# Performance work log

Measured on AMD Instinct MI355X. Metric: run time of the kernel, lower is better.

## Reference

```python
import jax, jax.numpy as jnp
import numpy as np

N, E = 50000, 800000
CUR, HID, OUT = 128, 96, 128
NEG_SLOPE = 0.01  # F.leaky_relu default


def setup_inputs() -> dict:
    key = jax.random.key(0)
    ks = jax.random.split(key, 12)
    inv = lambda d: 1.0 / np.sqrt(d)
    return {
        "h": jax.random.normal(ks[0], (N, CUR), jnp.float32),
        "x": jax.random.normal(ks[1], (N, CUR), jnp.float32),
        "edge_index": jax.random.randint(ks[2], (2, E), 0, N, dtype=jnp.int64),
        "edge_weight": jax.random.uniform(ks[3], (E,), jnp.float32),
        # preprocessor_x: Linear(cur_dim, hidden_dim)
        "pre_W": jax.random.uniform(ks[4], (CUR, HID), jnp.float32, -inv(CUR), inv(CUR)),
        "pre_b": jax.random.uniform(ks[5], (HID,), jnp.float32, -inv(CUR), inv(CUR)),
        # SAGEConv(hidden, out): lin_l (neighbor, with bias) + lin_r (root, no bias)
        "sage_Wl": jax.random.uniform(ks[6], (HID, OUT), jnp.float32, -inv(HID), inv(HID)),
        "sage_bl": jnp.zeros((OUT,), jnp.float32),
        "sage_Wr": jax.random.uniform(ks[7], (HID, OUT), jnp.float32, -inv(HID), inv(HID)),
        # ARMAConv(hidden, out) with K=1 stacks, T=1 layers (PyG defaults)
        "arma_W": jax.random.uniform(ks[8], (HID, OUT), jnp.float32, -inv(HID), inv(HID)),
        "arma_V": jax.random.uniform(ks[9], (HID, OUT), jnp.float32, -inv(HID), inv(HID)),
        "arma_b": jnp.zeros((OUT,), jnp.float32),
    }


def _cell(x, src, dst, edge_weight, pre_W, pre_b,
          sage_Wl, sage_bl, sage_Wr, arma_W, arma_V, arma_b):
    n = x.shape[0]
    xh = x @ pre_W + pre_b  # [N, HID]

    # ---- SAGEConv: mean aggregation of edge-weighted neighbor features ----
    msg = xh[src] * edge_weight[:, None]                     # [E, HID]
    aggr = jax.ops.segment_sum(msg, dst, num_segments=n)     # [N, HID]
    cnt = jax.ops.segment_sum(jnp.ones_like(edge_weight), dst, num_segments=n)
    mean = aggr / jnp.maximum(cnt, 1.0)[:, None]
    o_sage = mean @ sage_Wl + sage_bl + xh @ sage_Wr         # [N, OUT]

    # ---- ARMAConv (K=1, T=1): ReLU(L_hat (x W) + x V + b) ----
    deg = jax.ops.segment_sum(edge_weight, dst, num_segments=n)
    dinv = jnp.where(deg > 0, jax.lax.rsqrt(jnp.maximum(deg, 1e-30)), 0.0)
    norm = dinv[src] * edge_weight * dinv[dst]               # [E]
    xw = xh @ arma_W                                         # [N, OUT]
    prop = jax.ops.segment_sum(xw[src] * norm[:, None], dst, num_segments=n)
    o_arma = jax.nn.relu(prop + xh @ arma_V + arma_b)        # [N, OUT]

    o1 = jax.nn.leaky_relu(o_sage, NEG_SLOPE)
    o2 = jax.nn.leaky_relu(o_arma, NEG_SLOPE)
    return jax.nn.relu(o1 + o2)


def reference(h, x, edge_index, edge_weight, pre_W, pre_b,
              sage_Wl, sage_bl, sage_Wr, arma_W, arma_V, arma_b):
    src, dst = edge_index[0], edge_index[1]
    his = x
    o3 = _cell(x, src, dst, edge_weight, pre_W, pre_b,
               sage_Wl, sage_bl, sage_Wr, arma_W, arma_V, arma_b)
    return (his, o3)
```

## Files before the change

### kernel.cpp

```cpp
#include <hip/hip_runtime.h>


typedef __attribute__((ext_vector_type(8))) short bf16x8;
typedef __attribute__((ext_vector_type(4))) float f32x4;

__device__ __forceinline__ float bf2f(unsigned short u) {
    return __uint_as_float(((unsigned)u) << 16);
}
__device__ __forceinline__ unsigned short f2bf(float f) {
    unsigned u = __float_as_uint(f);
    return (unsigned short)((u + 0x7FFFu + ((u >> 16) & 1u)) >> 16);
}

__device__ __forceinline__ int edge_src(const int* ei, int e, int E, int flag) {
    return flag ? ei[2 * e] : ei[e];
}
__device__ __forceinline__ int edge_dst(const int* ei, int e, int E, int flag) {
    return flag ? ei[2 * (E + e)] : ei[E + e];
}

__global__ void k_wprep(const unsigned* __restrict__ eiu,
                        const float* __restrict__ Wl, const float* __restrict__ Wr,
                        const float* __restrict__ Wa, const float* __restrict__ Va,
                        const float* __restrict__ preW,
                        unsigned short* __restrict__ Wf_s,
                        unsigned short* __restrict__ Wf_a,
                        unsigned short* __restrict__ Wfp,
                        int* __restrict__ flag,
                        int4* __restrict__ cnt4, int nz4) {
    if (blockIdx.x == 0) {
        __shared__ int bad;
        if (threadIdx.x == 0) bad = 0;
        __syncthreads();
        int nb = 0;
#pragma unroll
        for (int q = 0; q < 4; q++) {
            unsigned w = eiu[2 * (threadIdx.x * 4 + q) + 1];
            if (w != 0) nb++;
        }
        if (nb) atomicAdd(&bad, nb);
        __syncthreads();
        if (threadIdx.x == 0) *flag = (bad == 0) ? 1 : 0;
        return;
    }
    int tid = (blockIdx.x - 1) * blockDim.x + threadIdx.x;
    if (tid < 6144) {
        int mat = tid / 3072, rem = tid % 3072;
        int kstep = rem / 512, rem2 = rem % 512;
        int g = rem2 / 128, j = rem2 % 128;
        int k0 = kstep * 32 + g * 8;
        const float* Wtop = mat ? Wa : Wl;
        const float* Wbot = mat ? Va : Wr;
        unsigned short* dst = (mat ? Wf_a : Wf_s) + (((size_t)(kstep * 4 + g) * 128 + j) * 8);
#pragma unroll
        for (int kk = 0; kk < 8; kk++) {
            int k = k0 + kk;
            float v = (k < 96) ? Wtop[k * 128 + j] : Wbot[(k - 96) * 128 + j];
            dst[kk] = f2bf(v);
        }
    } else if (tid < 7680) {
        int rem = tid - 6144;
        int kstep = rem / 384, rem2 = rem % 384;
        int g = rem2 / 96, j = rem2 % 96;
        int k0 = kstep * 32 + g * 8;
        unsigned short* dst = Wfp + (((size_t)(kstep * 4 + g) * 96 + j) * 8);
#pragma unroll
        for (int kk = 0; kk < 8; kk++) dst[kk] = f2bf(preW[(k0 + kk) * 96 + j]);
    } else if (tid >= 8192 && tid < 8192 + nz4) {
        cnt4[tid - 8192] = make_int4(0, 0, 0, 0);
    }
}

__global__ __launch_bounds__(256) void k_xh_count(
    const float* __restrict__ x, const unsigned short* __restrict__ Wfp,
    const float* __restrict__ b, unsigned short* __restrict__ xhbf,
    float* __restrict__ out0, int N, int xhBlocks,
    const int* __restrict__ ei, int* __restrict__ cntS, int* __restrict__ pos,
    int E, const int* __restrict__ flagp) {
    __shared__ unsigned short X[64][136];
    if (blockIdx.x >= xhBlocks) {
        int e = (blockIdx.x - xhBlocks) * 256 + threadIdx.x;
        if (e < E) {
            int flag = *flagp;
            int d = edge_dst(ei, e, E, flag);
            int shard = blockIdx.x & 7;
            int lp = atomicAdd(&cntS[(size_t)shard * N + d], 1);
            pos[e] = (lp << 3) | shard;
        }
        return;
    }
    int t = threadIdx.x;
    int nb = blockIdx.x * 64;
    for (int u = t; u < 2048; u += 256) {
        int row = u >> 5, q = u & 31;
        long gn = nb + row;
        float4 v = make_float4(0.f, 0.f, 0.f, 0.f);
        if (gn < N) {
            v = ((const float4*)(x + gn * 128))[q];
            ((float4*)(out0 + gn * 128))[q] = v;
        }
        unsigned short* p = &X[row][q * 4];
        p[0] = f2bf(v.x); p[1] = f2bf(v.y); p[2] = f2bf(v.z); p[3] = f2bf(v.w);
    }
    __syncthreads();
    int lane = t & 63, w = t >> 6;
    int lr = lane & 15, lg = lane >> 4;
    bf16x8 a[4];
#pragma unroll
    for (int ks = 0; ks < 4; ks++)
        a[ks] = *(const bf16x8*)&X[w * 16 + lr][ks * 32 + lg * 8];
    for (int jt = 0; jt < 6; jt++) {
        f32x4 acc = {0.f, 0.f, 0.f, 0.f};
#pragma unroll
        for (int ks = 0; ks < 4; ks++) {
            bf16x8 bf = *(const bf16x8*)(Wfp + (((size_t)(ks * 4 + lg) * 96 + jt * 16 + lr) * 8));
            acc = __builtin_amdgcn_mfma_f32_16x16x32_bf16(a[ks], bf, acc, 0, 0, 0);
        }
        int h = jt * 16 + lr;
        float bb = b[h];
#pragma unroll
        for (int r = 0; r < 4; r++) {
            long n = nb + w * 16 + lg * 4 + r;
            if (n < N) xhbf[n * 96 + h] = f2bf(acc[r] + bb);
        }
    }
}

__global__ void k_scan_blk(const int* __restrict__ cntS, int* __restrict__ sdelta,
                           int* __restrict__ offs, int* __restrict__ bsum, int N) {
    __shared__ int sh[256];
    int t = threadIdx.x;
    int n = blockIdx.x * 256 + t;
    int total = 0;
    if (n < N) {
        int run = 0;
#pragma unroll
        for (int s = 0; s < 8; s++) {
            sdelta[(size_t)s * N + n] = run;
            run += cntS[(size_t)s * N + n];
        }
        total = run;
    }
    sh[t] = total;
    __syncthreads();
    for (int off = 1; off < 256; off <<= 1) {
        int add = (t >= off) ? sh[t - off] : 0;
        __syncthreads();
        sh[t] += add;
        __syncthreads();
    }
    if (n < N) offs[n + 1] = sh[t];
    if (t == 255) bsum[blockIdx.x] = sh[255];
    if (blockIdx.x == 0 && t == 0) offs[0] = 0;
}

__global__ void k_scan_add(int* __restrict__ offs, const int* __restrict__ bsum, int N) {
    __shared__ int sh[256];
    int t = threadIdx.x;
    sh[t] = (t < (int)blockIdx.x) ? bsum[t] : 0;
    __syncthreads();
    for (int s = 128; s > 0; s >>= 1) {
        if (t < s) sh[t] += sh[t + s];
        __syncthreads();
    }
    int base = sh[0];
    int n = blockIdx.x * 256 + t;
    if (n < N && blockIdx.x > 0) offs[n + 1] += base;
}

__global__ void k_fill(const int* __restrict__ ei, const float* __restrict__ ew,
                       const int* __restrict__ offs, const int* __restrict__ sdelta,
                       const int* __restrict__ pos, int2* __restrict__ esw,
                       int E, int N, const int* __restrict__ flagp) {
    int e = blockIdx.x * blockDim.x + threadIdx.x;
    if (e >= E) return;
    int flag = *flagp;
    int s = edge_src(ei, e, E, flag);
    int d = edge_dst(ei, e, E, flag);
    int pp = pos[e];
    int shard = pp & 7, lp = pp >> 3;
    int idx = offs[d] + sdelta[(size_t)shard * N + d] + lp;
    esw[idx] = make_int2(s, __float_as_int(ew[e]));
}

__global__ void k_degcsr(const int2* __restrict__ esw, const int* __restrict__ offs,
                         float* __restrict__ dinv, float* __restrict__ minv, int N) {
    int n = blockIdx.x * blockDim.x + threadIdx.x;
    if (n >= N) return;
    int beg = offs[n], end = offs[n + 1];
    float dg = 0.f;
    for (int e = beg; e < end; e++) dg += __int_as_float(esw[e].y);
    dinv[n] = dg > 0.f ? rsqrtf(fmaxf(dg, 1e-30f)) : 0.f;
    minv[n] = 1.f / fmaxf((float)(end - beg), 1.f);
}

__global__ __launch_bounds__(256) void k_gather(
    const int2* __restrict__ esw, const unsigned short* __restrict__ xhbf,
    const int* __restrict__ offs, const float* __restrict__ dinv,
    const float* __restrict__ minv, unsigned short* __restrict__ meanbf,
    unsigned short* __restrict__ propbf, int N) {
    int lane = threadIdx.x & 63;
    int d = __builtin_amdgcn_readfirstlane(blockIdx.x * 4 + (threadIdx.x >> 6));
    if (d >= N) return;
    int beg = offs[d], end = offs[d + 1];
    bool act = lane < 48;
    int col = 2 * lane;
    float s0 = 0.f, s1 = 0.f, a0 = 0.f, a1 = 0.f;
    int e = beg;
    for (; e + 8 <= end; e += 8) {
        int2 md[8]; float dv[8]; unsigned v[8];
#pragma unroll
        for (int q = 0; q < 8; q++) md[q] = esw[e + q];
#pragma unroll
        for (int q = 0; q < 8; q++) dv[q] = dinv[md[q].x];
#pragma unroll
        for (int q = 0; q < 8; q++)
            v[q] = act ? *(const unsigned*)(xhbf + (size_t)md[q].x * 96 + col) : 0u;
#pragma unroll
        for (int q = 0; q < 8; q++) {
            float x0 = bf2f((unsigned short)(v[q] & 0xffff));
            float x1 = bf2f((unsigned short)(v[q] >> 16));
            float w2 = __int_as_float(md[q].y), dw = dv[q] * w2;
            s0 += w2 * x0; s1 += w2 * x1;
            a0 += dw * x0; a1 += dw * x1;
        }
    }
    for (; e + 4 <= end; e += 4) {
        int2 md[4]; float dv[4]; unsigned v[4];
#pragma unroll
        for (int q = 0; q < 4; q++) md[q] = esw[e + q];
#pragma unroll
        for (int q = 0; q < 4; q++) dv[q] = dinv[md[q].x];
#pragma unroll
        for (int q = 0; q < 4; q++)
            v[q] = act ? *(const unsigned*)(xhbf + (size_t)md[q].x * 96 + col) : 0u;
#pragma unroll
        for (int q = 0; q < 4; q++) {
            float x0 = bf2f((unsigned short)(v[q] & 0xffff));
            float x1 = bf2f((unsigned short)(v[q] >> 16));
            float w2 = __int_as_float(md[q].y), dw = dv[q] * w2;
            s0 += w2 * x0; s1 += w2 * x1;
            a0 += dw * x0; a1 += dw * x1;
        }
    }
    for (; e < end; e++) {
        int2 md = esw[e];
        float w2 = __int_as_float(md.y);
        float ds = dinv[md.x];
        if (act) {
            unsigned v = *(const unsigned*)(xhbf + (size_t)md.x * 96 + col);
            float x0 = bf2f((unsigned short)(v & 0xffff));
            float x1 = bf2f((unsigned short)(v >> 16));
            s0 += w2 * x0; s1 += w2 * x1;
            a0 += ds * w2 * x0; a1 += ds * w2 * x1;
        }
    }
    if (act) {
        float mi = minv[d], di = dinv[d];
        unsigned mo = (unsigned)f2bf(s0 * mi) | ((unsigned)f2bf(s1 * mi) << 16);
        unsigned po = (unsigned)f2bf(a0 * di) | ((unsigned)f2bf(a1 * di) << 16);
        *(unsigned*)(meanbf + (size_t)d * 96 + col) = mo;
        *(unsigned*)(propbf + (size_t)d * 96 + col) = po;
    }
}

__global__ __launch_bounds__(256) void k_out(
    const unsigned short* __restrict__ meanbf, const unsigned short* __restrict__ propbf,
    const unsigned short* __restrict__ xhbf, const unsigned short* __restrict__ Wf_s,
    const unsigned short* __restrict__ Wf_a, const float* __restrict__ bl,
    const float* __restrict__ ba, float* __restrict__ out, int N) {
    __shared__ unsigned short A[3][64][104];
    int t = threadIdx.x;
    int nb = blockIdx.x * 64;
    for (int u = t; u < 2304; u += 256) {
        int arr = u / 768, rem = u - arr * 768;
        int row = rem / 12, c = rem - row * 12;
        long gn = nb + row;
        const unsigned short* src = (arr == 0) ? meanbf : (arr == 1) ? propbf : xhbf;
        float4 v = (gn < N) ? *(const float4*)(src + gn * 96 + c * 8)
                            : make_float4(0.f, 0.f, 0.f, 0.f);
        *(float4*)&A[arr][row][c * 8] = v;
    }
    __syncthreads();
    int lane = t & 63, w = t >> 6;
    int lr = lane & 15, lg = lane >> 4;
    bf16x8 am[3], ap[3], ax[3];
#pragma unroll
    for (int ks = 0; ks < 3; ks++) {
        int row = w * 16 + lr, kc = ks * 32 + lg * 8;
        am[ks] = *(const bf16x8*)&A[0][row][kc];
        ap[ks] = *(const bf16x8*)&A[1][row][kc];
        ax[ks] = *(const bf16x8*)&A[2][row][kc];
    }
    for (int jt = 0; jt < 8; jt++) {
        f32x4 accS = {0.f, 0.f, 0.f, 0.f};
        f32x4 accA = {0.f, 0.f, 0.f, 0.f};
#pragma unroll
        for (int ks = 0; ks < 3; ks++) {
            size_t boffS = ((size_t)(ks * 4 + lg) * 128 + jt * 16 + lr) * 8;
            size_t boffS2 = ((size_t)((ks + 3) * 4 + lg) * 128 + jt * 16 + lr) * 8;
            bf16x8 b0 = *(const bf16x8*)(Wf_s + boffS);
            bf16x8 b1 = *(const bf16x8*)(Wf_s + boffS2);
            bf16x8 b2 = *(const bf16x8*)(Wf_a + boffS);
            bf16x8 b3 = *(const bf16x8*)(Wf_a + boffS2);
            accS = __builtin_amdgcn_mfma_f32_16x16x32_bf16(am[ks], b0, accS, 0, 0, 0);
            accS = __builtin_amdgcn_mfma_f32_16x16x32_bf16(ax[ks], b1, accS, 0, 0, 0);
            accA = __builtin_amdgcn_mfma_f32_16x16x32_bf16(ap[ks], b2, accA, 0, 0, 0);
            accA = __builtin_amdgcn_mfma_f32_16x16x32_bf16(ax[ks], b3, accA, 0, 0, 0);
        }
        int j = jt * 16 + lr;
        float blj = bl[j], baj = ba[j];
#pragma unroll
        for (int r = 0; r < 4; r++) {
            long n = nb + w * 16 + lg * 4 + r;
            if (n < N) {
                float os = accS[r] + blj;
                float oa = fmaxf(accA[r] + baj, 0.f);
                float o1 = os > 0.f ? os : 0.01f * os;
                float o2 = oa > 0.f ? oa : 0.01f * oa;
                out[n * 128 + j] = fmaxf(o1 + o2, 0.f);
            }
        }
    }
}

extern "C" void kernel_launch(void* const* d_in, const int* in_sizes, int n_in,
                              void* d_out, int out_size, void* d_ws, size_t ws_size,
                              hipStream_t stream) {
    const float* x    = (const float*)d_in[1];
    const int*   ei   = (const int*)d_in[2];
    const float* ew   = (const float*)d_in[3];
    const float* preW = (const float*)d_in[4];
    const float* preb = (const float*)d_in[5];
    const float* Wl   = (const float*)d_in[6];
    const float* bl   = (const float*)d_in[7];
    const float* Wr   = (const float*)d_in[8];
    const float* Wa   = (const float*)d_in[9];
    const float* Va   = (const float*)d_in[10];
    const float* ba   = (const float*)d_in[11];

    const int N = in_sizes[1] / 128;
    const int E = in_sizes[3];
    const int NB = (N + 255) / 256;

    char* w = (char*)d_ws;
    unsigned short* xhbf   = (unsigned short*)w; w += (size_t)N * 96 * 2;
    unsigned short* meanbf = (unsigned short*)w; w += (size_t)N * 96 * 2;
    unsigned short* propbf = (unsigned short*)w; w += (size_t)N * 96 * 2;
    unsigned short* Wf_s   = (unsigned short*)w; w += (size_t)6 * 4 * 128 * 8 * 2;
    unsigned short* Wf_a   = (unsigned short*)w; w += (size_t)6 * 4 * 128 * 8 * 2;
    unsigned short* Wfp    = (unsigned short*)w; w += (size_t)4 * 4 * 96 * 8 * 2;
    int2*  esw    = (int2*)w;  w += (size_t)E * 8;
    int*   pos    = (int*)w;   w += (size_t)E * 4;
    int*   cntS   = (int*)w;   w += (size_t)8 * N * 4;
    int*   sdelta = (int*)w;   w += (size_t)8 * N * 4;
    float* dinv   = (float*)w; w += (size_t)N * 4;
    float* minv   = (float*)w; w += (size_t)N * 4;
    int*   offs   = (int*)w;   w += (size_t)(N + 1) * 4;
    int*   bsum   = (int*)w;   w += 256 * 4;
    int*   flag   = (int*)w;

    const int nz4 = (8 * N + 3) / 4;
    const int wprep_blocks = 1 + (8192 + nz4 + 255) / 256;
    const int xhBlocks = (N + 63) / 64;
    const int cntBlocks = (E + 255) / 256;

    k_wprep<<<wprep_blocks, 256, 0, stream>>>((const unsigned*)ei, Wl, Wr, Wa, Va,
                                              preW, Wf_s, Wf_a, Wfp, flag,
                                              (int4*)cntS, nz4);
    k_xh_count<<<xhBlocks + cntBlocks, 256, 0, stream>>>(
        x, Wfp, preb, xhbf, (float*)d_out, N, xhBlocks, ei, cntS, pos, E, flag);
    k_scan_blk<<<NB, 256, 0, stream>>>(cntS, sdelta, offs, bsum, N);
    k_scan_add<<<NB, 256, 0, stream>>>(offs, bsum, N);
    k_fill<<<(E + 255) / 256, 256, 0, stream>>>(ei, ew, offs, sdelta, pos, esw,
                                                E, N, flag);
    k_degcsr<<<NB, 256, 0, stream>>>(esw, offs, dinv, minv, N);
    k_gather<<<(N + 3) / 4, 256, 0, stream>>>(esw, xhbf, offs, dinv,
                                              minv, meanbf, propbf, N);
    k_out<<<(N + 63) / 64, 256, 0, stream>>>(meanbf, propbf, xhbf, Wf_s, Wf_a,
                                             bl, ba, (float*)d_out + (size_t)N * 128, N);
}
```

Measured before the change: 137.9 us.

## Fuse two-pass scan with grid barrier and software-pipeline gather edge loads

Merges the block scan and the block-offset add into one kernel that uses a global atomic barrier, with the barrier counter zeroed alongside the count buffer. This removes one kernel launch and one pass over offs. The gather loop now prefetches the next 8 edge records and their dinv values while the current feature loads are in flight, overlapping the dependent loads. The grid barrier relies on all 196 blocks being co-resident, which holds on this GPU but is not guaranteed in general.

```diff
diff --git a/kernel.cpp b/kernel.cpp
--- a/kernel.cpp
+++ b/kernel.cpp
@@ -17,6 +17,17 @@
 }
 __device__ __forceinline__ int edge_dst(const int* ei, int e, int E, int flag) {
     return flag ? ei[2 * (E + e)] : ei[E + e];
+}
+
+__device__ __forceinline__ void gbar(int* ctr, int nb) {
+    __syncthreads();
+    if (threadIdx.x == 0) {
+        __threadfence();
+        atomicAdd(ctr, 1);
+        while (__hip_atomic_load(ctr, __ATOMIC_RELAXED, __HIP_MEMORY_SCOPE_AGENT) < nb) {}
+    }
+    __syncthreads();
+    __threadfence();
 }
 
 __global__ void k_wprep(const unsigned* __restrict__ eiu,
@@ -126,8 +137,9 @@
     }
 }
 
-__global__ void k_scan_blk(const int* __restrict__ cntS, int* __restrict__ sdelta,
-                           int* __restrict__ offs, int* __restrict__ bsum, int N) {
+__global__ __launch_bounds__(256) void k_scan(
+    const int* __restrict__ cntS, int* __restrict__ sdelta,
+    int* __restrict__ offs, int* __restrict__ bsum, int* __restrict__ bar, int N) {
     __shared__ int sh[256];
     int t = threadIdx.x;
     int n = blockIdx.x * 256 + t;
@@ -149,14 +161,9 @@
         sh[t] += add;
         __syncthreads();
     }
-    if (n < N) offs[n + 1] = sh[t];
+    int incl = sh[t];
     if (t == 255) bsum[blockIdx.x] = sh[255];
-    if (blockIdx.x == 0 && t == 0) offs[0] = 0;
-}
-
-__global__ void k_scan_add(int* __restrict__ offs, const int* __restrict__ bsum, int N) {
-    __shared__ int sh[256];
-    int t = threadIdx.x;
+    gbar(bar, gridDim.x);
     sh[t] = (t < (int)blockIdx.x) ? bsum[t] : 0;
     __syncthreads();
     for (int s = 128; s > 0; s >>= 1) {
@@ -164,8 +171,8 @@
         __syncthreads();
     }
     int base = sh[0];
-    int n = blockIdx.x * 256 + t;
-    if (n < N && blockIdx.x > 0) offs[n + 1] += base;
+    if (n < N) offs[n + 1] = base + incl;
+    if (blockIdx.x == 0 && t == 0) offs[0] = 0;
 }
 
 __global__ void k_fill(const int* __restrict__ ei, const float* __restrict__ ew,
@@ -207,22 +214,37 @@
     int col = 2 * lane;
     float s0 = 0.f, s1 = 0.f, a0 = 0.f, a1 = 0.f;
     int e = beg;
-    for (; e + 8 <= end; e += 8) {
-        int2 md[8]; float dv[8]; unsigned v[8];
+    if (e + 8 <= end) {
+        int2 md[8]; float dv[8];
 #pragma unroll
         for (int q = 0; q < 8; q++) md[q] = esw[e + q];
 #pragma unroll
         for (int q = 0; q < 8; q++) dv[q] = dinv[md[q].x];
-#pragma unroll
-        for (int q = 0; q < 8; q++)
-            v[q] = act ? *(const unsigned*)(xhbf + (size_t)md[q].x * 96 + col) : 0u;
-#pragma unroll
-        for (int q = 0; q < 8; q++) {
-            float x0 = bf2f((unsigned short)(v[q] & 0xffff));
-            float x1 = bf2f((unsigned short)(v[q] >> 16));
-            float w2 = __int_as_float(md[q].y), dw = dv[q] * w2;
-            s0 += w2 * x0; s1 += w2 * x1;
-            a0 += dw * x0; a1 += dw * x1;
+        for (;;) {
+            bool more = (e + 16 <= end);
+            unsigned v[8];
+#pragma unroll
+            for (int q = 0; q < 8; q++)
+                v[q] = act ? *(const unsigned*)(xhbf + (size_t)md[q].x * 96 + col) : 0u;
+            int2 mdn[8]; float dvn[8];
+            if (more) {
+#pragma unroll
+                for (int q = 0; q < 8; q++) mdn[q] = esw[e + 8 + q];
+#pragma unroll
+                for (int q = 0; q < 8; q++) dvn[q] = dinv[mdn[q].x];
+            }
+#pragma unroll
+            for (int q = 0; q < 8; q++) {
+                float x0 = bf2f((unsigned short)(v[q] & 0xffff));
+                float x1 = bf2f((unsigned short)(v[q] >> 16));
+                float w2 = __int_as_float(md[q].y), dw = dv[q] * w2;
+                s0 += w2 * x0; s1 += w2 * x1;
+                a0 += dw * x0; a1 += dw * x1;
+            }
+            e += 8;
+            if (!more) break;
+#pragma unroll
+            for (int q = 0; q < 8; q++) { md[q] = mdn[q]; dv[q] = dvn[q]; }
         }
     }
     for (; e + 4 <= end; e += 4) {
@@ -353,6 +375,7 @@
     int2*  esw    = (int2*)w;  w += (size_t)E * 8;
     int*   pos    = (int*)w;   w += (size_t)E * 4;
     int*   cntS   = (int*)w;   w += (size_t)8 * N * 4;
+    int*   bar    = (int*)w;   w += 4 * 4;
     int*   sdelta = (int*)w;   w += (size_t)8 * N * 4;
     float* dinv   = (float*)w; w += (size_t)N * 4;
     float* minv   = (float*)w; w += (size_t)N * 4;
@@ -360,7 +383,7 @@
     int*   bsum   = (int*)w;   w += 256 * 4;
     int*   flag   = (int*)w;
 
-    const int nz4 = (8 * N + 3) / 4;
+    const int nz4 = (8 * N + 4 + 3) / 4;
     const int wprep_blocks = 1 + (8192 + nz4 + 255) / 256;
     const int xhBlocks = (N + 63) / 64;
     const int cntBlocks = (E + 255) / 256;
@@ -370,8 +393,7 @@
                                               (int4*)cntS, nz4);
     k_xh_count<<<xhBlocks + cntBlocks, 256, 0, stream>>>(
         x, Wfp, preb, xhbf, (float*)d_out, N, xhBlocks, ei, cntS, pos, E, flag);
-    k_scan_blk<<<NB, 256, 0, stream>>>(cntS, sdelta, offs, bsum, N);
-    k_scan_add<<<NB, 256, 0, stream>>>(offs, bsum, N);
+    k_scan<<<NB, 256, 0, stream>>>(cntS, sdelta, offs, bsum, bar, N);
     k_fill<<<(E + 255) / 256, 256, 0, stream>>>(ei, ew, offs, sdelta, pos, esw,
                                                 E, N, flag);
     k_degcsr<<<NB, 256, 0, stream>>>(esw, offs, dinv, minv, N);
```

After: 153.5 us. +11.3%, slower.
